# Kernel optimization log

Measured on AMD Instinct MI355X. Metric: run time of the kernel, lower is better.

The kernel has to match this reference:

```python
import jax, jax.numpy as jnp
import numpy as np

D, P, R, K = 1024, 256, 64, 1024  # directions, sampling points, rank, subcarriers

def setup_inputs() -> dict:
    key = jax.random.key(0)
    k1, k2, k3 = jax.random.split(key, 3)
    return {
        "attenuation_vectors": jax.random.normal(k1, (D, P, R), dtype=jnp.float32),
        "radiation_vectors": jax.random.normal(k2, (D, P, R), dtype=jnp.float32),
        "frequency_basis_vectors": jax.random.normal(k3, (K, R), dtype=jnp.float32),
    }

def reference(attenuation_vectors, radiation_vectors, frequency_basis_vectors):
    # Original (per ray d, per subcarrier k):
    #   atten_factor[d,k] = sum_p sum_r u_rho[d,p,r] * F[k,r]
    #   rad_factor[d,k]   = sum_p sum_r u_s[d,p,r]   * F[k,r]
    #   csi[k] = (1/D) * sum_d atten_factor[d,k] * rad_factor[d,k]
    # Vectorized as two contractions over (p, r) plus a reduction over d.
    A = jnp.einsum('dpr,kr->dk', attenuation_vectors, frequency_basis_vectors)
    B = jnp.einsum('dpr,kr->dk', radiation_vectors, frequency_basis_vectors)
    num_directions = attenuation_vectors.shape[0]
    csi = jnp.sum(A * B, axis=0) / num_directions  # [K]
    return csi
```

## Files before the change

kernel.cpp:

```cpp
#include <hip/hip_runtime.h>

#define D_DIRS 1024
#define P_PTS  256
#define R_RANK 64
#define K_SUB  1024

typedef float v4f __attribute__((ext_vector_type(4)));

#define WS_A 0
#define WS_B (D_DIRS * R_RANK)
#define WS_MSUM (2 * D_DIRS * R_RANK)
#define NB_B 32
#define DCHUNK (D_DIRS / NB_B)

__device__ __forceinline__ v4f ntload(const v4f* __restrict__ p) {
    return __builtin_nontemporal_load(p);
}

__device__ __forceinline__ v4f shfl_xor_v4(v4f v, int m) {
    v4f r;
    r.x = __shfl_xor(v.x, m);
    r.y = __shfl_xor(v.y, m);
    r.z = __shfl_xor(v.z, m);
    r.w = __shfl_xor(v.w, m);
    return r;
}

__global__ __launch_bounds__(512) void k_reduce_p(const float* __restrict__ atten,
                                                  const float* __restrict__ rad,
                                                  float* __restrict__ ws) {
    const int t    = threadIdx.x;
    const int wave = t >> 6;
    const int lane = t & 63;
    const int d    = blockIdx.x * 4 + (wave >> 1);
    const int half = wave & 1;
    const int r4g  = lane & 7;
    const int pr   = lane >> 3;

    if (blockIdx.x == 0) {
        v4f z = {0.f, 0.f, 0.f, 0.f};
        ((v4f*)(ws + WS_MSUM))[t]       = z;
        ((v4f*)(ws + WS_MSUM))[t + 512] = z;
    }

    const int base = pr * 16 + half * 8 + r4g;
    const v4f* A4 = (const v4f*)atten + (size_t)d * 4096 + base;
    const v4f* B4 = (const v4f*)rad   + (size_t)d * 4096 + base;

    v4f pa[8], pb[8], na[8], nb[8];
#pragma unroll
    for (int j = 0; j < 8; ++j) pa[j] = ntload(A4 + j * 128);
#pragma unroll
    for (int j = 0; j < 8; ++j) pb[j] = ntload(B4 + j * 128);

    v4f acc_a = {0.f, 0.f, 0.f, 0.f};
    v4f acc_b = {0.f, 0.f, 0.f, 0.f};

#pragma unroll
    for (int mc = 0; mc < 4; ++mc) {
        if (mc < 3) {
            const int off = (mc + 1) * 8 * 128;
#pragma unroll
            for (int j = 0; j < 8; ++j) na[j] = ntload(A4 + off + j * 128);
#pragma unroll
            for (int j = 0; j < 8; ++j) nb[j] = ntload(B4 + off + j * 128);
        }
        acc_a = acc_a + (((pa[0] + pa[1]) + (pa[2] + pa[3])) +
                         ((pa[4] + pa[5]) + (pa[6] + pa[7])));
        acc_b = acc_b + (((pb[0] + pb[1]) + (pb[2] + pb[3])) +
                         ((pb[4] + pb[5]) + (pb[6] + pb[7])));
#pragma unroll
        for (int j = 0; j < 8; ++j) { pa[j] = na[j]; pb[j] = nb[j]; }
    }

    acc_a = acc_a + shfl_xor_v4(acc_a, 8);
    acc_a = acc_a + shfl_xor_v4(acc_a, 16);
    acc_a = acc_a + shfl_xor_v4(acc_a, 32);
    acc_b = acc_b + shfl_xor_v4(acc_b, 8);
    acc_b = acc_b + shfl_xor_v4(acc_b, 16);
    acc_b = acc_b + shfl_xor_v4(acc_b, 32);

    if (pr == 0) {
        ((v4f*)(ws + WS_A))[d * 16 + half * 8 + r4g] = acc_a;
        ((v4f*)(ws + WS_B))[d * 16 + half * 8 + r4g] = acc_b;
    }
}

__global__ __launch_bounds__(256) void k_partial_m(float* __restrict__ ws) {
    const int bb = blockIdx.x;
    const int t  = threadIdx.x;

    __shared__ float sa[DCHUNK * R_RANK];
    __shared__ float sb[DCHUNK * R_RANK];

    const float4* a4 = (const float4*)(ws + WS_A) + bb * (DCHUNK * R_RANK / 4);
    const float4* b4 = (const float4*)(ws + WS_B) + bb * (DCHUNK * R_RANK / 4);
    float4* sa4 = (float4*)sa;
    float4* sb4 = (float4*)sb;
    sa4[t]       = a4[t];
    sa4[t + 256] = a4[t + 256];
    sb4[t]       = b4[t];
    sb4[t + 256] = b4[t + 256];
    __syncthreads();

    const int c  = t & 63;
    const int wg = t >> 6;

    float acc[16];
#pragma unroll
    for (int i = 0; i < 16; ++i) acc[i] = 0.f;

    for (int dd = 0; dd < DCHUNK; ++dd) {
        const float bv = sb[dd * 64 + c];
        const float4* ar = (const float4*)&sa[dd * 64 + wg * 16];
        const float4 a0 = ar[0], a1 = ar[1], a2 = ar[2], a3 = ar[3];
        acc[0]  += a0.x * bv; acc[1]  += a0.y * bv; acc[2]  += a0.z * bv; acc[3]  += a0.w * bv;
        acc[4]  += a1.x * bv; acc[5]  += a1.y * bv; acc[6]  += a1.z * bv; acc[7]  += a1.w * bv;
        acc[8]  += a2.x * bv; acc[9]  += a2.y * bv; acc[10] += a2.z * bv; acc[11] += a2.w * bv;
        acc[12] += a3.x * bv; acc[13] += a3.y * bv; acc[14] += a3.z * bv; acc[15] += a3.w * bv;
    }

    float* Msum = ws + WS_MSUM;
#pragma unroll
    for (int i = 0; i < 16; ++i)
        atomicAdd(&Msum[(wg * 16 + i) * 64 + c], acc[i]);
}

__global__ __launch_bounds__(256) void k_csi(const float* __restrict__ ws,
                                             const float* __restrict__ freq,
                                             float* __restrict__ out) {
    const int bb = blockIdx.x;
    const int t  = threadIdx.x;

    __shared__ float Ms[64 * 68];
    __shared__ float Fs[64 * 65];
    __shared__ float red[4][64];

    const float4* M4 = (const float4*)(ws + WS_MSUM);
#pragma unroll
    for (int i = 0; i < 4; ++i) {
        const int idx4 = i * 256 + t;
        const float4 s = M4[idx4];
        const int r = idx4 >> 4, c4 = idx4 & 15;
        *(float4*)&Ms[r * 68 + c4 * 4] = s;
    }

    const float4* F4 = (const float4*)freq + bb * 1024;
#pragma unroll
    for (int i = 0; i < 4; ++i) {
        const int idx4 = i * 256 + t;
        const float4 v = F4[idx4];
        const int row = idx4 >> 4, c4 = idx4 & 15;
        Fs[row * 65 + c4 * 4 + 0] = v.x;
        Fs[row * 65 + c4 * 4 + 1] = v.y;
        Fs[row * 65 + c4 * 4 + 2] = v.z;
        Fs[row * 65 + c4 * 4 + 3] = v.w;
    }
    __syncthreads();

    const int kl = t & 63;
    const int jg = t >> 6;

    float h[16];
#pragma unroll
    for (int j = 0; j < 16; ++j) h[j] = 0.f;

    for (int r = 0; r < 64; ++r) {
        const float fv = Fs[kl * 65 + r];
        const float4* mr = (const float4*)&Ms[r * 68 + jg * 16];
        const float4 m0 = mr[0], m1 = mr[1], m2 = mr[2], m3 = mr[3];
        h[0]  += fv * m0.x; h[1]  += fv * m0.y; h[2]  += fv * m0.z; h[3]  += fv * m0.w;
        h[4]  += fv * m1.x; h[5]  += fv * m1.y; h[6]  += fv * m1.z; h[7]  += fv * m1.w;
        h[8]  += fv * m2.x; h[9]  += fv * m2.y; h[10] += fv * m2.z; h[11] += fv * m2.w;
        h[12] += fv * m3.x; h[13] += fv * m3.y; h[14] += fv * m3.z; h[15] += fv * m3.w;
    }

    float part = 0.f;
#pragma unroll
    for (int j = 0; j < 16; ++j) part += h[j] * Fs[kl * 65 + jg * 16 + j];

    red[jg][kl] = part;
    __syncthreads();
    if (t < 64) {
        out[bb * 64 + t] =
            (red[0][t] + red[1][t] + red[2][t] + red[3][t]) * (1.0f / (float)D_DIRS);
    }
}

extern "C" void kernel_launch(void* const* d_in, const int* in_sizes, int n_in,
                              void* d_out, int out_size, void* d_ws, size_t ws_size,
                              hipStream_t stream) {
    const float* atten = (const float*)d_in[0];
    const float* rad   = (const float*)d_in[1];
    const float* freq  = (const float*)d_in[2];
    float* out = (float*)d_out;
    float* ws  = (float*)d_ws;

    k_reduce_p<<<D_DIRS / 4, 512, 0, stream>>>(atten, rad, ws);
    k_partial_m<<<NB_B, 256, 0, stream>>>(ws);
    k_csi<<<16, 256, 0, stream>>>(ws, freq, out);
}
```

Baseline: 147.4 us.

## Remap reduce_p to one block per direction with full-row wave loads

The p-reduction kernel is reorganised so each 256-thread block handles a single direction. Each wave covers a contiguous quarter of the points, and each lane loads a full row of 16 float4s, so a wave reads 1 KB contiguous per load. Per-thread loads drop from 16 to 8 per stage, and partial sums are combined across waves through shared memory with a block barrier. The aim is more blocks and better coalescing for this bandwidth-bound stream over 2 GB of input, at the cost of an extra LDS reduction and sync.

```diff
diff --git a/kernel.cpp b/kernel.cpp
--- a/kernel.cpp
+++ b/kernel.cpp
@@ -26,63 +26,68 @@
     return r;
 }
 
-__global__ __launch_bounds__(512) void k_reduce_p(const float* __restrict__ atten,
-                                                  const float* __restrict__ rad,
-                                                  float* __restrict__ ws) {
+__global__ __launch_bounds__(256, 4) void k_reduce_p(const float* __restrict__ atten,
+                                                     const float* __restrict__ rad,
+                                                     float* __restrict__ ws) {
     const int t    = threadIdx.x;
     const int wave = t >> 6;
     const int lane = t & 63;
-    const int d    = blockIdx.x * 4 + (wave >> 1);
-    const int half = wave & 1;
-    const int r4g  = lane & 7;
-    const int pr   = lane >> 3;
+    const int pr   = lane >> 4;
+    const int r4g  = lane & 15;
+    const int d    = blockIdx.x;
 
     if (blockIdx.x == 0) {
         v4f z = {0.f, 0.f, 0.f, 0.f};
-        ((v4f*)(ws + WS_MSUM))[t]       = z;
-        ((v4f*)(ws + WS_MSUM))[t + 512] = z;
-    }
-
-    const int base = pr * 16 + half * 8 + r4g;
+#pragma unroll
+        for (int i = 0; i < 4; ++i)
+            ((v4f*)(ws + WS_MSUM))[t + i * 256] = z;
+    }
+
+    const int base = wave * 1024 + pr * 16 + r4g;
     const v4f* A4 = (const v4f*)atten + (size_t)d * 4096 + base;
     const v4f* B4 = (const v4f*)rad   + (size_t)d * 4096 + base;
 
-    v4f pa[8], pb[8], na[8], nb[8];
-#pragma unroll
-    for (int j = 0; j < 8; ++j) pa[j] = ntload(A4 + j * 128);
-#pragma unroll
-    for (int j = 0; j < 8; ++j) pb[j] = ntload(B4 + j * 128);
+    v4f pa[4], pb[4], na[4], nb[4];
+#pragma unroll
+    for (int j = 0; j < 4; ++j) pa[j] = ntload(A4 + j * 64);
+#pragma unroll
+    for (int j = 0; j < 4; ++j) pb[j] = ntload(B4 + j * 64);
 
     v4f acc_a = {0.f, 0.f, 0.f, 0.f};
     v4f acc_b = {0.f, 0.f, 0.f, 0.f};
 
 #pragma unroll
-    for (int mc = 0; mc < 4; ++mc) {
-        if (mc < 3) {
-            const int off = (mc + 1) * 8 * 128;
-#pragma unroll
-            for (int j = 0; j < 8; ++j) na[j] = ntload(A4 + off + j * 128);
-#pragma unroll
-            for (int j = 0; j < 8; ++j) nb[j] = ntload(B4 + off + j * 128);
+    for (int c = 0; c < 4; ++c) {
+        if (c < 3) {
+            const int off = (c + 1) * 256;
+#pragma unroll
+            for (int j = 0; j < 4; ++j) na[j] = ntload(A4 + off + j * 64);
+#pragma unroll
+            for (int j = 0; j < 4; ++j) nb[j] = ntload(B4 + off + j * 64);
         }
-        acc_a = acc_a + (((pa[0] + pa[1]) + (pa[2] + pa[3])) +
-                         ((pa[4] + pa[5]) + (pa[6] + pa[7])));
-        acc_b = acc_b + (((pb[0] + pb[1]) + (pb[2] + pb[3])) +
-                         ((pb[4] + pb[5]) + (pb[6] + pb[7])));
-#pragma unroll
-        for (int j = 0; j < 8; ++j) { pa[j] = na[j]; pb[j] = nb[j]; }
-    }
-
-    acc_a = acc_a + shfl_xor_v4(acc_a, 8);
+        acc_a = acc_a + ((pa[0] + pa[1]) + (pa[2] + pa[3]));
+        acc_b = acc_b + ((pb[0] + pb[1]) + (pb[2] + pb[3]));
+#pragma unroll
+        for (int j = 0; j < 4; ++j) { pa[j] = na[j]; pb[j] = nb[j]; }
+    }
+
     acc_a = acc_a + shfl_xor_v4(acc_a, 16);
     acc_a = acc_a + shfl_xor_v4(acc_a, 32);
-    acc_b = acc_b + shfl_xor_v4(acc_b, 8);
     acc_b = acc_b + shfl_xor_v4(acc_b, 16);
     acc_b = acc_b + shfl_xor_v4(acc_b, 32);
 
-    if (pr == 0) {
-        ((v4f*)(ws + WS_A))[d * 16 + half * 8 + r4g] = acc_a;
-        ((v4f*)(ws + WS_B))[d * 16 + half * 8 + r4g] = acc_b;
+    __shared__ v4f sA[4][16];
+    __shared__ v4f sB[4][16];
+    if (lane < 16) {
+        sA[wave][r4g] = acc_a;
+        sB[wave][r4g] = acc_b;
+    }
+    __syncthreads();
+    if (t < 16) {
+        v4f a = (sA[0][t] + sA[1][t]) + (sA[2][t] + sA[3][t]);
+        v4f b = (sB[0][t] + sB[1][t]) + (sB[2][t] + sB[3][t]);
+        ((v4f*)(ws + WS_A))[d * 16 + t] = a;
+        ((v4f*)(ws + WS_B))[d * 16 + t] = b;
     }
 }
 
@@ -196,7 +201,7 @@
     float* out = (float*)d_out;
     float* ws  = (float*)d_ws;
 
-    k_reduce_p<<<D_DIRS / 4, 512, 0, stream>>>(atten, rad, ws);
+    k_reduce_p<<<D_DIRS, 256, 0, stream>>>(atten, rad, ws);
     k_partial_m<<<NB_B, 256, 0, stream>>>(ws);
     k_csi<<<16, 256, 0, stream>>>(ws, freq, out);
 }
```

New measurement: 148.0 us. About the same (+0.4%).

## Fuse three kernels into one cooperative kernel with grid-wide syncs

Applied to the files above, without the earlier changes.

Merges the p-reduction, partial outer-product accumulation and final CSI contraction into a single cooperative launch of 256 blocks, separated by grid barriers. The aim is to remove two kernel launch gaps and the tail overhead between stages. Later stages are remapped to 512-thread blocks with fewer accumulators per thread. The cost is two grid-wide syncs, and blocks idle during the small later stages. The launch also depends on cooperative co-residency of all 256 blocks.

```diff
diff --git a/kernel.cpp b/kernel.cpp
--- a/kernel.cpp
+++ b/kernel.cpp
@@ -1,4 +1,7 @@
 #include <hip/hip_runtime.h>
+#include <hip/hip_cooperative_groups.h>
+
+namespace cg = cooperative_groups;
 
 #define D_DIRS 1024
 #define P_PTS  256
@@ -26,164 +29,162 @@
     return r;
 }
 
-__global__ __launch_bounds__(512) void k_reduce_p(const float* __restrict__ atten,
-                                                  const float* __restrict__ rad,
-                                                  float* __restrict__ ws) {
+__global__ __launch_bounds__(512) void k_fused(const float* __restrict__ atten,
+                                               const float* __restrict__ rad,
+                                               const float* __restrict__ freq,
+                                               float* __restrict__ ws,
+                                               float* __restrict__ out) {
     const int t    = threadIdx.x;
+    const int bid  = blockIdx.x;
     const int wave = t >> 6;
     const int lane = t & 63;
-    const int d    = blockIdx.x * 4 + (wave >> 1);
-    const int half = wave & 1;
-    const int r4g  = lane & 7;
-    const int pr   = lane >> 3;
-
-    if (blockIdx.x == 0) {
-        v4f z = {0.f, 0.f, 0.f, 0.f};
-        ((v4f*)(ws + WS_MSUM))[t]       = z;
-        ((v4f*)(ws + WS_MSUM))[t + 512] = z;
+
+    __shared__ float smem[64 * 68 + 64 * 65 + 8 * 64];
+
+    {
+        const int d    = bid * 4 + (wave >> 1);
+        const int half = wave & 1;
+        const int r4g  = lane & 7;
+        const int pr   = lane >> 3;
+
+        if (bid == 0) {
+            v4f z = {0.f, 0.f, 0.f, 0.f};
+            ((v4f*)(ws + WS_MSUM))[t]       = z;
+            ((v4f*)(ws + WS_MSUM))[t + 512] = z;
+        }
+
+        const int base = pr * 16 + half * 8 + r4g;
+        const v4f* A4 = (const v4f*)atten + (size_t)d * 4096 + base;
+        const v4f* B4 = (const v4f*)rad   + (size_t)d * 4096 + base;
+
+        v4f pa[8], pb[8], na[8], nb[8];
+#pragma unroll
+        for (int j = 0; j < 8; ++j) pa[j] = ntload(A4 + j * 128);
+#pragma unroll
+        for (int j = 0; j < 8; ++j) pb[j] = ntload(B4 + j * 128);
+
+        v4f acc_a = {0.f, 0.f, 0.f, 0.f};
+        v4f acc_b = {0.f, 0.f, 0.f, 0.f};
+
+#pragma unroll
+        for (int mc = 0; mc < 4; ++mc) {
+            if (mc < 3) {
+                const int off = (mc + 1) * 8 * 128;
+#pragma unroll
+                for (int j = 0; j < 8; ++j) na[j] = ntload(A4 + off + j * 128);
+#pragma unroll
+                for (int j = 0; j < 8; ++j) nb[j] = ntload(B4 + off + j * 128);
+            }
+            acc_a = acc_a + (((pa[0] + pa[1]) + (pa[2] + pa[3])) +
+                             ((pa[4] + pa[5]) + (pa[6] + pa[7])));
+            acc_b = acc_b + (((pb[0] + pb[1]) + (pb[2] + pb[3])) +
+                             ((pb[4] + pb[5]) + (pb[6] + pb[7])));
+#pragma unroll
+            for (int j = 0; j < 8; ++j) { pa[j] = na[j]; pb[j] = nb[j]; }
+        }
+
+        acc_a = acc_a + shfl_xor_v4(acc_a, 8);
+        acc_a = acc_a + shfl_xor_v4(acc_a, 16);
+        acc_a = acc_a + shfl_xor_v4(acc_a, 32);
+        acc_b = acc_b + shfl_xor_v4(acc_b, 8);
+        acc_b = acc_b + shfl_xor_v4(acc_b, 16);
+        acc_b = acc_b + shfl_xor_v4(acc_b, 32);
+
+        if (pr == 0) {
+            ((v4f*)(ws + WS_A))[d * 16 + half * 8 + r4g] = acc_a;
+            ((v4f*)(ws + WS_B))[d * 16 + half * 8 + r4g] = acc_b;
+        }
     }
 
-    const int base = pr * 16 + half * 8 + r4g;
-    const v4f* A4 = (const v4f*)atten + (size_t)d * 4096 + base;
-    const v4f* B4 = (const v4f*)rad   + (size_t)d * 4096 + base;
-
-    v4f pa[8], pb[8], na[8], nb[8];
-#pragma unroll
-    for (int j = 0; j < 8; ++j) pa[j] = ntload(A4 + j * 128);
-#pragma unroll
-    for (int j = 0; j < 8; ++j) pb[j] = ntload(B4 + j * 128);
-
-    v4f acc_a = {0.f, 0.f, 0.f, 0.f};
-    v4f acc_b = {0.f, 0.f, 0.f, 0.f};
-
-#pragma unroll
-    for (int mc = 0; mc < 4; ++mc) {
-        if (mc < 3) {
-            const int off = (mc + 1) * 8 * 128;
-#pragma unroll
-            for (int j = 0; j < 8; ++j) na[j] = ntload(A4 + off + j * 128);
-#pragma unroll
-            for (int j = 0; j < 8; ++j) nb[j] = ntload(B4 + off + j * 128);
-        }
-        acc_a = acc_a + (((pa[0] + pa[1]) + (pa[2] + pa[3])) +
-                         ((pa[4] + pa[5]) + (pa[6] + pa[7])));
-        acc_b = acc_b + (((pb[0] + pb[1]) + (pb[2] + pb[3])) +
-                         ((pb[4] + pb[5]) + (pb[6] + pb[7])));
-#pragma unroll
-        for (int j = 0; j < 8; ++j) { pa[j] = na[j]; pb[j] = nb[j]; }
+    cg::this_grid().sync();
+
+    if (bid < NB_B) {
+        float* sa = smem;
+        float* sb = smem + DCHUNK * R_RANK;
+
+        const float4* a4 = (const float4*)(ws + WS_A) + bid * (DCHUNK * R_RANK / 4);
+        const float4* b4 = (const float4*)(ws + WS_B) + bid * (DCHUNK * R_RANK / 4);
+        ((float4*)sa)[t] = a4[t];
+        ((float4*)sb)[t] = b4[t];
+        __syncthreads();
+
+        const int c  = t & 63;
+        const int wg = t >> 6;
+
+        float acc[8];
+#pragma unroll
+        for (int i = 0; i < 8; ++i) acc[i] = 0.f;
+
+        for (int dd = 0; dd < DCHUNK; ++dd) {
+            const float bv = sb[dd * 64 + c];
+            const float4* ar = (const float4*)&sa[dd * 64 + wg * 8];
+            const float4 a0 = ar[0], a1 = ar[1];
+            acc[0] += a0.x * bv; acc[1] += a0.y * bv; acc[2] += a0.z * bv; acc[3] += a0.w * bv;
+            acc[4] += a1.x * bv; acc[5] += a1.y * bv; acc[6] += a1.z * bv; acc[7] += a1.w * bv;
+        }
+
+        float* Msum = ws + WS_MSUM;
+#pragma unroll
+        for (int i = 0; i < 8; ++i)
+            atomicAdd(&Msum[(wg * 8 + i) * 64 + c], acc[i]);
     }
 
-    acc_a = acc_a + shfl_xor_v4(acc_a, 8);
-    acc_a = acc_a + shfl_xor_v4(acc_a, 16);
-    acc_a = acc_a + shfl_xor_v4(acc_a, 32);
-    acc_b = acc_b + shfl_xor_v4(acc_b, 8);
-    acc_b = acc_b + shfl_xor_v4(acc_b, 16);
-    acc_b = acc_b + shfl_xor_v4(acc_b, 32);
-
-    if (pr == 0) {
-        ((v4f*)(ws + WS_A))[d * 16 + half * 8 + r4g] = acc_a;
-        ((v4f*)(ws + WS_B))[d * 16 + half * 8 + r4g] = acc_b;
-    }
-}
-
-__global__ __launch_bounds__(256) void k_partial_m(float* __restrict__ ws) {
-    const int bb = blockIdx.x;
-    const int t  = threadIdx.x;
-
-    __shared__ float sa[DCHUNK * R_RANK];
-    __shared__ float sb[DCHUNK * R_RANK];
-
-    const float4* a4 = (const float4*)(ws + WS_A) + bb * (DCHUNK * R_RANK / 4);
-    const float4* b4 = (const float4*)(ws + WS_B) + bb * (DCHUNK * R_RANK / 4);
-    float4* sa4 = (float4*)sa;
-    float4* sb4 = (float4*)sb;
-    sa4[t]       = a4[t];
-    sa4[t + 256] = a4[t + 256];
-    sb4[t]       = b4[t];
-    sb4[t + 256] = b4[t + 256];
-    __syncthreads();
-
-    const int c  = t & 63;
-    const int wg = t >> 6;
-
-    float acc[16];
-#pragma unroll
-    for (int i = 0; i < 16; ++i) acc[i] = 0.f;
-
-    for (int dd = 0; dd < DCHUNK; ++dd) {
-        const float bv = sb[dd * 64 + c];
-        const float4* ar = (const float4*)&sa[dd * 64 + wg * 16];
-        const float4 a0 = ar[0], a1 = ar[1], a2 = ar[2], a3 = ar[3];
-        acc[0]  += a0.x * bv; acc[1]  += a0.y * bv; acc[2]  += a0.z * bv; acc[3]  += a0.w * bv;
-        acc[4]  += a1.x * bv; acc[5]  += a1.y * bv; acc[6]  += a1.z * bv; acc[7]  += a1.w * bv;
-        acc[8]  += a2.x * bv; acc[9]  += a2.y * bv; acc[10] += a2.z * bv; acc[11] += a2.w * bv;
-        acc[12] += a3.x * bv; acc[13] += a3.y * bv; acc[14] += a3.z * bv; acc[15] += a3.w * bv;
-    }
-
-    float* Msum = ws + WS_MSUM;
-#pragma unroll
-    for (int i = 0; i < 16; ++i)
-        atomicAdd(&Msum[(wg * 16 + i) * 64 + c], acc[i]);
-}
-
-__global__ __launch_bounds__(256) void k_csi(const float* __restrict__ ws,
-                                             const float* __restrict__ freq,
-                                             float* __restrict__ out) {
-    const int bb = blockIdx.x;
-    const int t  = threadIdx.x;
-
-    __shared__ float Ms[64 * 68];
-    __shared__ float Fs[64 * 65];
-    __shared__ float red[4][64];
-
-    const float4* M4 = (const float4*)(ws + WS_MSUM);
-#pragma unroll
-    for (int i = 0; i < 4; ++i) {
-        const int idx4 = i * 256 + t;
-        const float4 s = M4[idx4];
-        const int r = idx4 >> 4, c4 = idx4 & 15;
-        *(float4*)&Ms[r * 68 + c4 * 4] = s;
-    }
-
-    const float4* F4 = (const float4*)freq + bb * 1024;
-#pragma unroll
-    for (int i = 0; i < 4; ++i) {
-        const int idx4 = i * 256 + t;
-        const float4 v = F4[idx4];
-        const int row = idx4 >> 4, c4 = idx4 & 15;
-        Fs[row * 65 + c4 * 4 + 0] = v.x;
-        Fs[row * 65 + c4 * 4 + 1] = v.y;
-        Fs[row * 65 + c4 * 4 + 2] = v.z;
-        Fs[row * 65 + c4 * 4 + 3] = v.w;
-    }
-    __syncthreads();
-
-    const int kl = t & 63;
-    const int jg = t >> 6;
-
-    float h[16];
-#pragma unroll
-    for (int j = 0; j < 16; ++j) h[j] = 0.f;
-
-    for (int r = 0; r < 64; ++r) {
-        const float fv = Fs[kl * 65 + r];
-        const float4* mr = (const float4*)&Ms[r * 68 + jg * 16];
-        const float4 m0 = mr[0], m1 = mr[1], m2 = mr[2], m3 = mr[3];
-        h[0]  += fv * m0.x; h[1]  += fv * m0.y; h[2]  += fv * m0.z; h[3]  += fv * m0.w;
-        h[4]  += fv * m1.x; h[5]  += fv * m1.y; h[6]  += fv * m1.z; h[7]  += fv * m1.w;
-        h[8]  += fv * m2.x; h[9]  += fv * m2.y; h[10] += fv * m2.z; h[11] += fv * m2.w;
-        h[12] += fv * m3.x; h[13] += fv * m3.y; h[14] += fv * m3.z; h[15] += fv * m3.w;
-    }
-
-    float part = 0.f;
-#pragma unroll
-    for (int j = 0; j < 16; ++j) part += h[j] * Fs[kl * 65 + jg * 16 + j];
-
-    red[jg][kl] = part;
-    __syncthreads();
-    if (t < 64) {
-        out[bb * 64 + t] =
-            (red[0][t] + red[1][t] + red[2][t] + red[3][t]) * (1.0f / (float)D_DIRS);
+    cg::this_grid().sync();
+
+    if (bid < 16) {
+        float* Ms  = smem;
+        float* Fs  = smem + 64 * 68;
+        float* red = smem + 64 * 68 + 64 * 65;
+
+        const float4* M4 = (const float4*)(ws + WS_MSUM);
+#pragma unroll
+        for (int i = 0; i < 2; ++i) {
+            const int idx4 = i * 512 + t;
+            const float4 s = M4[idx4];
+            const int r = idx4 >> 4, c4 = idx4 & 15;
+            *(float4*)&Ms[r * 68 + c4 * 4] = s;
+        }
+
+        const float4* F4 = (const float4*)freq + bid * 1024;
+#pragma unroll
+        for (int i = 0; i < 2; ++i) {
+            const int idx4 = i * 512 + t;
+            const float4 v = F4[idx4];
+            const int row = idx4 >> 4, c4 = idx4 & 15;
+            Fs[row * 65 + c4 * 4 + 0] = v.x;
+            Fs[row * 65 + c4 * 4 + 1] = v.y;
+            Fs[row * 65 + c4 * 4 + 2] = v.z;
+            Fs[row * 65 + c4 * 4 + 3] = v.w;
+        }
+        __syncthreads();
+
+        const int kl = t & 63;
+        const int jg = t >> 6;
+
+        float h[8];
+#pragma unroll
+        for (int j = 0; j < 8; ++j) h[j] = 0.f;
+
+        for (int r = 0; r < 64; ++r) {
+            const float fv = Fs[kl * 65 + r];
+            const float4* mr = (const float4*)&Ms[r * 68 + jg * 8];
+            const float4 m0 = mr[0], m1 = mr[1];
+            h[0] += fv * m0.x; h[1] += fv * m0.y; h[2] += fv * m0.z; h[3] += fv * m0.w;
+            h[4] += fv * m1.x; h[5] += fv * m1.y; h[6] += fv * m1.z; h[7] += fv * m1.w;
+        }
+
+        float part = 0.f;
+#pragma unroll
+        for (int j = 0; j < 8; ++j) part += h[j] * Fs[kl * 65 + jg * 8 + j];
+
+        red[jg * 64 + kl] = part;
+        __syncthreads();
+        if (t < 64) {
+            float s = 0.f;
+#pragma unroll
+            for (int g = 0; g < 8; ++g) s += red[g * 64 + t];
+            out[bid * 64 + t] = s * (1.0f / (float)D_DIRS);
+        }
     }
 }
 
@@ -196,7 +197,7 @@
     float* out = (float*)d_out;
     float* ws  = (float*)d_ws;
 
-    k_reduce_p<<<D_DIRS / 4, 512, 0, stream>>>(atten, rad, ws);
-    k_partial_m<<<NB_B, 256, 0, stream>>>(ws);
-    k_csi<<<16, 256, 0, stream>>>(ws, freq, out);
-}
+    void* args[] = {(void*)&atten, (void*)&rad, (void*)&freq, (void*)&ws, (void*)&out};
+    hipLaunchCooperativeKernel((const void*)k_fused, dim3(D_DIRS / 4), dim3(512),
+                               args, 0, stream);
+}
```

New measurement: 208.4 us. 41.4% more time.

## Fuse outer-product accumulation into the streaming reduction kernel

Applied to the files above, without the earlier changes.

Each block now forms the 64x64 outer-product contribution of its four directions directly from shared memory and atomically adds it into the global M sum, which removes the separate partial-M kernel and its workspace round trip. Zeroing of the accumulator moves to a memset on the stream. In exchange there are 256 blocks each issuing 4096 atomics onto the same 4096 addresses, so contention could be heavy.

```diff
diff --git a/kernel.cpp b/kernel.cpp
--- a/kernel.cpp
+++ b/kernel.cpp
@@ -7,11 +7,7 @@
 
 typedef float v4f __attribute__((ext_vector_type(4)));
 
-#define WS_A 0
-#define WS_B (D_DIRS * R_RANK)
 #define WS_MSUM (2 * D_DIRS * R_RANK)
-#define NB_B 32
-#define DCHUNK (D_DIRS / NB_B)
 
 __device__ __forceinline__ v4f ntload(const v4f* __restrict__ p) {
     return __builtin_nontemporal_load(p);
@@ -26,7 +22,7 @@
     return r;
 }
 
-__global__ __launch_bounds__(512) void k_reduce_p(const float* __restrict__ atten,
+__global__ __launch_bounds__(512) void k_stream_m(const float* __restrict__ atten,
                                                   const float* __restrict__ rad,
                                                   float* __restrict__ ws) {
     const int t    = threadIdx.x;
@@ -36,12 +32,6 @@
     const int half = wave & 1;
     const int r4g  = lane & 7;
     const int pr   = lane >> 3;
-
-    if (blockIdx.x == 0) {
-        v4f z = {0.f, 0.f, 0.f, 0.f};
-        ((v4f*)(ws + WS_MSUM))[t]       = z;
-        ((v4f*)(ws + WS_MSUM))[t + 512] = z;
-    }
 
     const int base = pr * 16 + half * 8 + r4g;
     const v4f* A4 = (const v4f*)atten + (size_t)d * 4096 + base;
@@ -80,50 +70,38 @@
     acc_b = acc_b + shfl_xor_v4(acc_b, 16);
     acc_b = acc_b + shfl_xor_v4(acc_b, 32);
 
+    __shared__ float sa[4][64];
+    __shared__ float sb[4][64];
+
+    const int wp = wave >> 1;
     if (pr == 0) {
-        ((v4f*)(ws + WS_A))[d * 16 + half * 8 + r4g] = acc_a;
-        ((v4f*)(ws + WS_B))[d * 16 + half * 8 + r4g] = acc_b;
+        *(v4f*)&sa[wp][(half * 8 + r4g) * 4] = acc_a;
+        *(v4f*)&sb[wp][(half * 8 + r4g) * 4] = acc_b;
     }
-}
-
-__global__ __launch_bounds__(256) void k_partial_m(float* __restrict__ ws) {
-    const int bb = blockIdx.x;
-    const int t  = threadIdx.x;
-
-    __shared__ float sa[DCHUNK * R_RANK];
-    __shared__ float sb[DCHUNK * R_RANK];
-
-    const float4* a4 = (const float4*)(ws + WS_A) + bb * (DCHUNK * R_RANK / 4);
-    const float4* b4 = (const float4*)(ws + WS_B) + bb * (DCHUNK * R_RANK / 4);
-    float4* sa4 = (float4*)sa;
-    float4* sb4 = (float4*)sb;
-    sa4[t]       = a4[t];
-    sa4[t + 256] = a4[t + 256];
-    sb4[t]       = b4[t];
-    sb4[t + 256] = b4[t + 256];
     __syncthreads();
 
-    const int c  = t & 63;
-    const int wg = t >> 6;
+    const int row = t >> 3;
+    const int cb  = (t & 7) * 8;
 
-    float acc[16];
+    float acc[8];
 #pragma unroll
-    for (int i = 0; i < 16; ++i) acc[i] = 0.f;
+    for (int j = 0; j < 8; ++j) acc[j] = 0.f;
 
-    for (int dd = 0; dd < DCHUNK; ++dd) {
-        const float bv = sb[dd * 64 + c];
-        const float4* ar = (const float4*)&sa[dd * 64 + wg * 16];
-        const float4 a0 = ar[0], a1 = ar[1], a2 = ar[2], a3 = ar[3];
-        acc[0]  += a0.x * bv; acc[1]  += a0.y * bv; acc[2]  += a0.z * bv; acc[3]  += a0.w * bv;
-        acc[4]  += a1.x * bv; acc[5]  += a1.y * bv; acc[6]  += a1.z * bv; acc[7]  += a1.w * bv;
-        acc[8]  += a2.x * bv; acc[9]  += a2.y * bv; acc[10] += a2.z * bv; acc[11] += a2.w * bv;
-        acc[12] += a3.x * bv; acc[13] += a3.y * bv; acc[14] += a3.z * bv; acc[15] += a3.w * bv;
+#pragma unroll
+    for (int dd = 0; dd < 4; ++dd) {
+        const float av = sa[dd][row];
+        const float4 b0 = *(const float4*)&sb[dd][cb];
+        const float4 b1 = *(const float4*)&sb[dd][cb + 4];
+        acc[0] += av * b0.x; acc[1] += av * b0.y;
+        acc[2] += av * b0.z; acc[3] += av * b0.w;
+        acc[4] += av * b1.x; acc[5] += av * b1.y;
+        acc[6] += av * b1.z; acc[7] += av * b1.w;
     }
 
     float* Msum = ws + WS_MSUM;
 #pragma unroll
-    for (int i = 0; i < 16; ++i)
-        atomicAdd(&Msum[(wg * 16 + i) * 64 + c], acc[i]);
+    for (int j = 0; j < 8; ++j)
+        atomicAdd(&Msum[row * 64 + cb + j], acc[j]);
 }
 
 __global__ __launch_bounds__(256) void k_csi(const float* __restrict__ ws,
@@ -196,7 +174,7 @@
     float* out = (float*)d_out;
     float* ws  = (float*)d_ws;
 
-    k_reduce_p<<<D_DIRS / 4, 512, 0, stream>>>(atten, rad, ws);
-    k_partial_m<<<NB_B, 256, 0, stream>>>(ws);
+    hipMemsetAsync(ws + WS_MSUM, 0, R_RANK * R_RANK * sizeof(float), stream);
+    k_stream_m<<<D_DIRS / 4, 512, 0, stream>>>(atten, rad, ws);
     k_csi<<<16, 256, 0, stream>>>(ws, freq, out);
 }
```

Result: slower. 220.5 us (+49.6%).
